# Performance work log

Measured on AMD Instinct MI355X. Metric: run time of the kernel, lower is better.

The kernel has to match this reference:

```python
import jax, jax.numpy as jnp
import numpy as np

N = 100000   # nodes
E = 1000000  # edges
F_IN = 128
H = 256
G = 64       # graphs in batch
EPS = 1e-5   # BatchNorm eps


def setup_inputs() -> dict:
    key = jax.random.key(0)
    ks = jax.random.split(key, 16)
    s = 0.05
    d = {}
    d["x"] = jax.random.normal(ks[0], (N, F_IN), jnp.float32)
    d["edge_index"] = jax.random.randint(ks[1], (2, E), 0, N, dtype=jnp.int32)
    d["batch"] = jnp.sort(jax.random.randint(ks[2], (N,), 0, G, dtype=jnp.int32))
    # block1 (128 -> 256, has projection)
    d["W1"] = jax.random.normal(ks[3], (F_IN, H), jnp.float32) * s
    d["b1"] = jnp.zeros((H,), jnp.float32)
    d["g1"] = jnp.ones((H,), jnp.float32)
    d["be1"] = jnp.zeros((H,), jnp.float32)
    d["P1"] = jax.random.normal(ks[4], (F_IN, H), jnp.float32) * s
    # blocks 2-4 (256 -> 256)
    for i, k in zip((2, 3, 4), (ks[5], ks[6], ks[7])):
        d[f"W{i}"] = jax.random.normal(k, (H, H), jnp.float32) * s
        d[f"b{i}"] = jnp.zeros((H,), jnp.float32)
        d[f"g{i}"] = jnp.ones((H,), jnp.float32)
        d[f"be{i}"] = jnp.zeros((H,), jnp.float32)
    d["Wl"] = jax.random.normal(ks[8], (H, 1), jnp.float32) * s
    d["bl"] = jnp.zeros((1,), jnp.float32)
    return d


def _gcn_norm(edge_index):
    # PyG gcn_norm: add self-loops, deg from dst column, norm = d^-1/2[src]*d^-1/2[dst]
    src, dst = edge_index[0], edge_index[1]
    deg = jax.ops.segment_sum(jnp.ones((E,), jnp.float32), dst, num_segments=N) + 1.0
    dis = jax.lax.rsqrt(deg)
    enorm = dis[src] * dis[dst]          # [E] normalization per edge
    self_w = 1.0 / deg                   # self-loop weight = deg^-1
    return src, dst, enorm, self_w


def _block(x, src, dst, enorm, self_w, W, b, g, be, P=None):
    hw = x @ W                                            # [N, H]
    msg = hw[src] * enorm[:, None]                        # [E, H] gather
    agg = jax.ops.segment_sum(msg, dst, num_segments=N)   # scatter-add
    agg = agg + hw * self_w[:, None] + b                  # self-loop + bias
    # BatchNorm1d (training-mode batch statistics, biased variance)
    m = jnp.mean(agg, axis=0)
    v = jnp.var(agg, axis=0)
    out = jax.nn.relu((agg - m) * jax.lax.rsqrt(v + EPS) * g + be)
    res = x @ P if P is not None else x
    return out + res


def reference(x, edge_index, batch, W1, b1, g1, be1, P1,
              W2, b2, g2, be2, W3, b3, g3, be3, W4, b4, g4, be4, Wl, bl):
    src, dst, enorm, self_w = _gcn_norm(edge_index)
    h = _block(x, src, dst, enorm, self_w, W1, b1, g1, be1, P1)
    h = _block(h, src, dst, enorm, self_w, W2, b2, g2, be2)
    h = _block(h, src, dst, enorm, self_w, W3, b3, g3, be3)
    h = _block(h, src, dst, enorm, self_w, W4, b4, g4, be4)
    # global mean pool over graphs
    sums = jax.ops.segment_sum(h, batch, num_segments=G)                       # [G, H]
    cnt = jax.ops.segment_sum(jnp.ones((N,), jnp.float32), batch, num_segments=G)
    pooled = sums / jnp.maximum(cnt, 1.0)[:, None]
    return pooled @ Wl + bl                                                    # [G, 1]
```

## Files before the change

kernel.cpp:

```cpp
#include <hip/hip_runtime.h>
#include <cstdint>
#include <cstddef>

#define NN 100000
#define NE 1000000
#define FIN 128
#define HD 256
#define NG 64
#define BNEPS 1e-5f

typedef unsigned short ushort_t;
typedef __attribute__((ext_vector_type(8))) short bf16x8;
typedef __attribute__((ext_vector_type(4))) float f32x4;


__device__ inline float b2f(unsigned short u) {
    union { float f; unsigned int i; } x; x.i = ((unsigned int)u) << 16; return x.f;
}
__device__ inline unsigned short f2b(float f) {
    union { float f; unsigned int i; } x; x.f = f;
    unsigned int r = x.i + 0x7FFFu + ((x.i >> 16) & 1u);
    return (unsigned short)(r >> 16);
}
__device__ inline float  ld1(const unsigned short* p) { return b2f(*p); }
__device__ inline float4 ld4v(const unsigned short* p) {
    ushort4 u = *(const ushort4*)p;
    return make_float4(b2f(u.x), b2f(u.y), b2f(u.z), b2f(u.w));
}
__device__ inline float2 ld2v(const unsigned short* p) {
    ushort2 u = *(const ushort2*)p;
    return make_float2(b2f(u.x), b2f(u.y));
}
__device__ inline void st4v(unsigned short* p, float4 v) {
    ushort4 u; u.x = f2b(v.x); u.y = f2b(v.y); u.z = f2b(v.z); u.w = f2b(v.w);
    *(ushort4*)p = u;
}
__device__ inline void st2v(unsigned short* p, float2 v) {
    ushort2 u; u.x = f2b(v.x); u.y = f2b(v.y);
    *(ushort2*)p = u;
}

__device__ inline void bn_sc_sh(float s, float q, float g, float be, float& sc, float& sh) {
    float m = s * (1.0f / NN);
    float v = q * (1.0f / NN) - m * m;
    sc = g * rsqrtf(v + BNEPS);
    sh = be - m * sc;
}


__global__ __launch_bounds__(256) void count_deg_k(const int* __restrict__ dst, int* __restrict__ cnt) {
    int e = blockIdx.x * 256 + threadIdx.x;
    if (e < NE) atomicAdd(&cnt[dst[e]], 1);
}

__global__ __launch_bounds__(256) void node_prep_k(const int* __restrict__ cnt,
                                                   float* __restrict__ dis, float* __restrict__ selfw) {
    int i = blockIdx.x * 256 + threadIdx.x;
    if (i < NN) {
        float d = (float)cnt[i] + 1.0f;
        dis[i] = rsqrtf(d);
        selfw[i] = 1.0f / d;
    }
}

__global__ __launch_bounds__(1024) void scan_reduce_k(const int* __restrict__ cnt, int* __restrict__ partials) {
    __shared__ int sh[1024];
    int i = blockIdx.x * 1024 + threadIdx.x;
    sh[threadIdx.x] = (i < NN) ? cnt[i] : 0;
    __syncthreads();
    for (int off = 512; off > 0; off >>= 1) {
        if (threadIdx.x < off) sh[threadIdx.x] += sh[threadIdx.x + off];
        __syncthreads();
    }
    if (threadIdx.x == 0) partials[blockIdx.x] = sh[0];
}

__global__ void scan_partials_k(int* partials, int nb) {
    if (threadIdx.x == 0 && blockIdx.x == 0) {
        int run = 0;
        for (int b = 0; b < nb; b++) { int v = partials[b]; partials[b] = run; run += v; }
    }
}

__global__ __launch_bounds__(1024) void scan_write_k(const int* __restrict__ cnt,
                                                     const int* __restrict__ partials,
                                                     int* __restrict__ rowptr) {
    __shared__ int sh[1024];
    int i = blockIdx.x * 1024 + threadIdx.x;
    int v = (i < NN) ? cnt[i] : 0;
    sh[threadIdx.x] = v;
    __syncthreads();
    for (int off = 1; off < 1024; off <<= 1) {
        int t = (threadIdx.x >= off) ? sh[threadIdx.x - off] : 0;
        __syncthreads();
        sh[threadIdx.x] += t;
        __syncthreads();
    }
    if (i < NN) rowptr[i] = partials[blockIdx.x] + sh[threadIdx.x] - v;
    if (i == NN - 1) rowptr[NN] = partials[blockIdx.x] + sh[threadIdx.x];
}

__global__ __launch_bounds__(256) void fill_csr_k(const int* __restrict__ src, const int* __restrict__ dst,
                                                  const int* __restrict__ rowptr, int* __restrict__ cursor,
                                                  const float* __restrict__ dis,
                                                  int2* __restrict__ csr) {
    int e = blockIdx.x * 256 + threadIdx.x;
    if (e < NE) {
        int d = dst[e], s = src[e];
        int pos = rowptr[d] + atomicAdd(&cursor[d], 1);
        float w = dis[s] * dis[d];
        csr[pos] = make_int2(s, __float_as_int(w));
    }
}

__global__ __launch_bounds__(256) void x2b_k(const float* __restrict__ x, unsigned short* __restrict__ xb) {
    int i = blockIdx.x * 256 + threadIdx.x;
    if (i < NN * FIN / 4) {
        float4 v = *reinterpret_cast<const float4*>(x + (size_t)i * 4);
        ushort4 u; u.x = f2b(v.x); u.y = f2b(v.y); u.z = f2b(v.z); u.w = f2b(v.w);
        *reinterpret_cast<ushort4*>(xb + (size_t)i * 4) = u;
    }
}

__global__ __launch_bounds__(256) void wt_all_k(const float* __restrict__ W1, const float* __restrict__ P1,
                                                const float* __restrict__ W2, const float* __restrict__ W3,
                                                const float* __restrict__ W4,
                                                unsigned short* __restrict__ w1t, unsigned short* __restrict__ p1t,
                                                unsigned short* __restrict__ w2t, unsigned short* __restrict__ w3t,
                                                unsigned short* __restrict__ w4t) {
    int b = blockIdx.x;
    const float* W; unsigned short* Bt; int K; int base;
    if (b < 128)      { W = W1; Bt = w1t; K = 128; base = b; }
    else if (b < 256) { W = P1; Bt = p1t; K = 128; base = b - 128; }
    else if (b < 512) { W = W2; Bt = w2t; K = 256; base = b - 256; }
    else if (b < 768) { W = W3; Bt = w3t; K = 256; base = b - 512; }
    else              { W = W4; Bt = w4t; K = 256; base = b - 768; }
    int i = base * 256 + threadIdx.x;
    if (i < K * 256) {
        int k = i >> 8, n = i & 255;
        Bt[n * K + k] = f2b(W[k * 256 + n]);
    }
}


template<int COLS>
__global__ __launch_bounds__(256) void spmm_k(const unsigned short* __restrict__ h,
                                              const int* __restrict__ rowptr,
                                              const int2* __restrict__ csr,
                                              const float* __restrict__ selfw,
                                              unsigned short* __restrict__ z) {
    const int lane = threadIdx.x & 63;
    const int row = blockIdx.x * 4 + (threadIdx.x >> 6);
    if (row >= NN) return;
    if constexpr (COLS == 256) {
        float4 a = ld4v(h + (size_t)row * COLS + lane * 4);
        float sw = selfw[row];
        float4 acc = make_float4(a.x * sw, a.y * sw, a.z * sw, a.w * sw);
        int e = rowptr[row];
        const int e1 = rowptr[row + 1];
        for (; e + 8 <= e1; e += 8) {
            int2 cc[8];
#pragma unroll
            for (int j = 0; j < 8; j++) cc[j] = csr[e + j];
            float4 hv[8];
#pragma unroll
            for (int j = 0; j < 8; j++) hv[j] = ld4v(h + (size_t)cc[j].x * COLS + lane * 4);
#pragma unroll
            for (int j = 0; j < 8; j++) {
                float w = __int_as_float(cc[j].y);
                acc.x += w * hv[j].x; acc.y += w * hv[j].y; acc.z += w * hv[j].z; acc.w += w * hv[j].w;
            }
        }
        for (; e + 4 <= e1; e += 4) {
            int2 c0 = csr[e], c1 = csr[e + 1], c2 = csr[e + 2], c3 = csr[e + 3];
            float4 h0 = ld4v(h + (size_t)c0.x * COLS + lane * 4);
            float4 h1 = ld4v(h + (size_t)c1.x * COLS + lane * 4);
            float4 h2 = ld4v(h + (size_t)c2.x * COLS + lane * 4);
            float4 h3 = ld4v(h + (size_t)c3.x * COLS + lane * 4);
            float w0 = __int_as_float(c0.y), w1 = __int_as_float(c1.y);
            float w2 = __int_as_float(c2.y), w3 = __int_as_float(c3.y);
            acc.x += w0 * h0.x; acc.y += w0 * h0.y; acc.z += w0 * h0.z; acc.w += w0 * h0.w;
            acc.x += w1 * h1.x; acc.y += w1 * h1.y; acc.z += w1 * h1.z; acc.w += w1 * h1.w;
            acc.x += w2 * h2.x; acc.y += w2 * h2.y; acc.z += w2 * h2.z; acc.w += w2 * h2.w;
            acc.x += w3 * h3.x; acc.y += w3 * h3.y; acc.z += w3 * h3.z; acc.w += w3 * h3.w;
        }
        for (; e < e1; e++) {
            int2 c = csr[e];
            float w = __int_as_float(c.y);
            float4 hv = ld4v(h + (size_t)c.x * COLS + lane * 4);
            acc.x += w * hv.x; acc.y += w * hv.y; acc.z += w * hv.z; acc.w += w * hv.w;
        }
        st4v(z + (size_t)row * COLS + lane * 4, acc);
    } else {
        float2 a = ld2v(h + (size_t)row * COLS + lane * 2);
        float sw = selfw[row];
        float2 acc = make_float2(a.x * sw, a.y * sw);
        int e = rowptr[row];
        const int e1 = rowptr[row + 1];
        for (; e + 8 <= e1; e += 8) {
            int2 cc[8];
#pragma unroll
            for (int j = 0; j < 8; j++) cc[j] = csr[e + j];
            float2 hv[8];
#pragma unroll
            for (int j = 0; j < 8; j++) hv[j] = ld2v(h + (size_t)cc[j].x * COLS + lane * 2);
#pragma unroll
            for (int j = 0; j < 8; j++) {
                float w = __int_as_float(cc[j].y);
                acc.x += w * hv[j].x; acc.y += w * hv[j].y;
            }
        }
        for (; e + 4 <= e1; e += 4) {
            int2 c0 = csr[e], c1 = csr[e + 1], c2 = csr[e + 2], c3 = csr[e + 3];
            float2 h0 = ld2v(h + (size_t)c0.x * COLS + lane * 2);
            float2 h1 = ld2v(h + (size_t)c1.x * COLS + lane * 2);
            float2 h2 = ld2v(h + (size_t)c2.x * COLS + lane * 2);
            float2 h3 = ld2v(h + (size_t)c3.x * COLS + lane * 2);
            float w0 = __int_as_float(c0.y), w1 = __int_as_float(c1.y);
            float w2 = __int_as_float(c2.y), w3 = __int_as_float(c3.y);
            acc.x += w0 * h0.x; acc.y += w0 * h0.y;
            acc.x += w1 * h1.x; acc.y += w1 * h1.y;
            acc.x += w2 * h2.x; acc.y += w2 * h2.y;
            acc.x += w3 * h3.x; acc.y += w3 * h3.y;
        }
        for (; e < e1; e++) {
            int2 c = csr[e];
            float w = __int_as_float(c.y);
            float2 hv = ld2v(h + (size_t)c.x * COLS + lane * 2);
            acc.x += w * hv.x; acc.y += w * hv.y;
        }
        st2v(z + (size_t)row * COLS + lane * 2, acc);
    }
}


#define RPB 391

template<int K, int MODE>
__global__ __launch_bounds__(1024, 4) void mgemm_k(const unsigned short* __restrict__ A,
                                                   const unsigned short* __restrict__ Bt,
                                                   const float* __restrict__ bias,
                                                   unsigned short* __restrict__ C,
                                                   const float* __restrict__ gamma,
                                                   const float* __restrict__ beta,
                                                   const float* __restrict__ sums_in,
                                                   const unsigned short* __restrict__ aggin,
                                                   float* __restrict__ sums_out, int M) {
    constexpr int NF = 8;
    constexpr int SEGS = K / 8;
    constexpr int KS = K / 32;
    __shared__ char Bl[256 * K * 2];
    __shared__ float sstat[512];
    const int tid  = threadIdx.x;
    const int lane = tid & 63;
    const int wid  = tid >> 6;
    const int wr   = wid & 7;
    const int cw   = wid >> 3;
    const int q    = lane >> 4;
    const int rl   = lane & 15;
    const int col0 = cw * 128;
    const int rbase = blockIdx.x * RPB;
    const int rend  = min(rbase + RPB, M);

    for (int s = tid; s < 256 * SEGS; s += 1024) {
        int col = s / SEGS, j = s % SEGS;
        uint4 v = *reinterpret_cast<const uint4*>(Bt + (size_t)col * K + j * 8);
        *reinterpret_cast<uint4*>(Bl + col * (K * 2) + ((j ^ (col & 7)) << 4)) = v;
    }
    if (MODE == 0 && tid < 512) sstat[tid] = 0.f;
    __syncthreads();

    for (int it = 0; it < 2; it++) {
        const int row0 = rbase + it * 256 + wr * 32;
        if (row0 >= rend) continue;

        const int a0r = min(row0 + rl, M - 1);
        const int a1r = min(row0 + 16 + rl, M - 1);
        const unsigned short* pa0 = A + (size_t)a0r * K + q * 8;
        const unsigned short* pa1 = A + (size_t)a1r * K + q * 8;

        f32x4 acc[2][NF];
#pragma unroll
        for (int m = 0; m < 2; m++)
#pragma unroll
            for (int n = 0; n < NF; n++) acc[m][n] = (f32x4){0.f, 0.f, 0.f, 0.f};

#pragma unroll
        for (int ks = 0; ks < KS; ks++) {
            bf16x8 af0 = *reinterpret_cast<const bf16x8*>(pa0 + ks * 32);
            bf16x8 af1 = *reinterpret_cast<const bf16x8*>(pa1 + ks * 32);
#pragma unroll
            for (int nf = 0; nf < NF; nf++) {
                int colL = col0 + nf * 16 + rl;
                bf16x8 bf = *reinterpret_cast<const bf16x8*>(Bl + colL * (K * 2) + (((ks * 4 + q) ^ (colL & 7)) << 4));
                acc[0][nf] = __builtin_amdgcn_mfma_f32_16x16x32_bf16(bf, af0, acc[0][nf], 0, 0, 0);
                acc[1][nf] = __builtin_amdgcn_mfma_f32_16x16x32_bf16(bf, af1, acc[1][nf], 0, 0, 0);
            }
        }

        const int g0 = row0 + rl, g1 = row0 + 16 + rl;
        const bool ok0 = g0 < rend, ok1 = g1 < rend;
#pragma unroll
        for (int nf = 0; nf < NF; nf++) {
            int cb = col0 + nf * 16 + q * 4;
            f32x4 v0 = acc[0][nf], v1 = acc[1][nf];
            if (MODE == 0) {
                float4 bb = *reinterpret_cast<const float4*>(bias + cb);
                v0[0] += bb.x; v0[1] += bb.y; v0[2] += bb.z; v0[3] += bb.w;
                v1[0] += bb.x; v1[1] += bb.y; v1[2] += bb.z; v1[3] += bb.w;
            } else {
                float4 s4 = *reinterpret_cast<const float4*>(sums_in + cb);
                float4 q4 = *reinterpret_cast<const float4*>(sums_in + 256 + cb);
                float4 gm = *reinterpret_cast<const float4*>(gamma + cb);
                float4 bt = *reinterpret_cast<const float4*>(beta + cb);
                float sc[4], sh[4];
                bn_sc_sh(s4.x, q4.x, gm.x, bt.x, sc[0], sh[0]);
                bn_sc_sh(s4.y, q4.y, gm.y, bt.y, sc[1], sh[1]);
                bn_sc_sh(s4.z, q4.z, gm.z, bt.z, sc[2], sh[2]);
                bn_sc_sh(s4.w, q4.w, gm.w, bt.w, sc[3], sh[3]);
                if (ok0) {
                    ushort4 ag = *reinterpret_cast<const ushort4*>(aggin + (size_t)g0 * HD + cb);
                    v0[0] += fmaxf(fmaf(b2f(ag.x), sc[0], sh[0]), 0.f);
                    v0[1] += fmaxf(fmaf(b2f(ag.y), sc[1], sh[1]), 0.f);
                    v0[2] += fmaxf(fmaf(b2f(ag.z), sc[2], sh[2]), 0.f);
                    v0[3] += fmaxf(fmaf(b2f(ag.w), sc[3], sh[3]), 0.f);
                }
                if (ok1) {
                    ushort4 ag = *reinterpret_cast<const ushort4*>(aggin + (size_t)g1 * HD + cb);
                    v1[0] += fmaxf(fmaf(b2f(ag.x), sc[0], sh[0]), 0.f);
                    v1[1] += fmaxf(fmaf(b2f(ag.y), sc[1], sh[1]), 0.f);
                    v1[2] += fmaxf(fmaf(b2f(ag.z), sc[2], sh[2]), 0.f);
                    v1[3] += fmaxf(fmaf(b2f(ag.w), sc[3], sh[3]), 0.f);
                }
            }
            if (ok0) {
                ushort4 u; u.x = f2b(v0[0]); u.y = f2b(v0[1]); u.z = f2b(v0[2]); u.w = f2b(v0[3]);
                *reinterpret_cast<ushort4*>(C + (size_t)g0 * HD + cb) = u;
            }
            if (ok1) {
                ushort4 u; u.x = f2b(v1[0]); u.y = f2b(v1[1]); u.z = f2b(v1[2]); u.w = f2b(v1[3]);
                *reinterpret_cast<ushort4*>(C + (size_t)g1 * HD + cb) = u;
            }
            if (MODE == 0) {
                if (!ok0) { v0[0] = v0[1] = v0[2] = v0[3] = 0.f; }
                if (!ok1) { v1[0] = v1[1] = v1[2] = v1[3] = 0.f; }
                float s[4], qq[4];
#pragma unroll
                for (int j = 0; j < 4; j++) {
                    s[j]  = v0[j] + v1[j];
                    qq[j] = v0[j] * v0[j] + v1[j] * v1[j];
                }
#pragma unroll
                for (int m = 1; m < 16; m <<= 1) {
#pragma unroll
                    for (int j = 0; j < 4; j++) {
                        s[j]  += __shfl_xor(s[j], m, 64);
                        qq[j] += __shfl_xor(qq[j], m, 64);
                    }
                }
                if (rl == 0) {
#pragma unroll
                    for (int j = 0; j < 4; j++) {
                        atomicAdd(&sstat[cb + j], s[j]);
                        atomicAdd(&sstat[256 + cb + j], qq[j]);
                    }
                }
            }
        }
    }

    if (MODE == 0) {
        __syncthreads();
        if (tid < 512) atomicAdd(&sums_out[tid], sstat[tid]);
    }
}


__global__ __launch_bounds__(256) void epi_k(const unsigned short* __restrict__ agg,
                                             const unsigned short* __restrict__ res,
                                             const float* __restrict__ sums,
                                             const float* __restrict__ gamma,
                                             const float* __restrict__ beta,
                                             unsigned short* __restrict__ out) {
    const size_t total = (size_t)NN * (HD / 4);
    size_t i = (size_t)blockIdx.x * 256 + threadIdx.x;
    const size_t stride = (size_t)gridDim.x * 256;
    for (; i < total; i += stride) {
        int cq = ((int)(i & 63)) * 4;
        float4 a = ld4v(agg + i * 4);
        float4 r = ld4v(res + i * 4);
        float4 s4 = *reinterpret_cast<const float4*>(sums + cq);
        float4 q4 = *reinterpret_cast<const float4*>(sums + 256 + cq);
        float4 gm = *reinterpret_cast<const float4*>(gamma + cq);
        float4 bt = *reinterpret_cast<const float4*>(beta + cq);
        float sc0, sh0, sc1, sh1, sc2, sh2, sc3, sh3;
        bn_sc_sh(s4.x, q4.x, gm.x, bt.x, sc0, sh0);
        bn_sc_sh(s4.y, q4.y, gm.y, bt.y, sc1, sh1);
        bn_sc_sh(s4.z, q4.z, gm.z, bt.z, sc2, sh2);
        bn_sc_sh(s4.w, q4.w, gm.w, bt.w, sc3, sh3);
        float4 o;
        o.x = fmaxf(fmaf(a.x, sc0, sh0), 0.f) + r.x;
        o.y = fmaxf(fmaf(a.y, sc1, sh1), 0.f) + r.y;
        o.z = fmaxf(fmaf(a.z, sc2, sh2), 0.f) + r.z;
        o.w = fmaxf(fmaf(a.w, sc3, sh3), 0.f) + r.w;
        st4v(out + i * 4, o);
    }
}


#define EP_RPB 40

__global__ __launch_bounds__(256) void epi_pool_k(const unsigned short* __restrict__ lin,
                                                  const unsigned short* __restrict__ res,
                                                  const float* __restrict__ sums,
                                                  const float* __restrict__ gamma,
                                                  const float* __restrict__ beta,
                                                  const int* __restrict__ batch,
                                                  float* __restrict__ pooled) {
    const int c = threadIdx.x;
    const int rs = blockIdx.x * EP_RPB;
    if (rs >= NN) return;
    const int re = min(rs + EP_RPB, NN);
    float sc, sh;
    bn_sc_sh(sums[c], sums[256 + c], gamma[c], beta[c], sc, sh);
    float acc = 0.f;
    int cur = batch[rs];
    int r = rs;
    for (; r + 4 <= re; r += 4) {
        float a[4], rr[4]; int g[4];
#pragma unroll
        for (int j = 0; j < 4; j++) {
            a[j]  = b2f(lin[(size_t)(r + j) * HD + c]);
            rr[j] = b2f(res[(size_t)(r + j) * HD + c]);
            g[j]  = batch[r + j];
        }
#pragma unroll
        for (int j = 0; j < 4; j++) {
            if (g[j] != cur) { atomicAdd(&pooled[(size_t)cur * HD + c], acc); acc = 0.f; cur = g[j]; }
            acc += fmaxf(fmaf(a[j], sc, sh), 0.f) + rr[j];
        }
    }
    for (; r < re; r++) {
        int g = batch[r];
        if (g != cur) { atomicAdd(&pooled[(size_t)cur * HD + c], acc); acc = 0.f; cur = g; }
        float a = b2f(lin[(size_t)r * HD + c]);
        float rv = b2f(res[(size_t)r * HD + c]);
        acc += fmaxf(fmaf(a, sc, sh), 0.f) + rv;
    }
    atomicAdd(&pooled[(size_t)cur * HD + c], acc);
}

__global__ void pool_out_k(const float* __restrict__ pooled, const int* __restrict__ batch,
                           const float* __restrict__ Wl, const float* __restrict__ bl,
                           float* __restrict__ out) {
    int g = threadIdx.x;
    if (g < NG) {
        auto lb = [&](int val) {
            int lo = 0, hi = NN;
            while (lo < hi) { int mid = (lo + hi) >> 1; if (batch[mid] < val) lo = mid + 1; else hi = mid; }
            return lo;
        };
        int c0 = lb(g), c1 = lb(g + 1);
        float cn = fmaxf((float)(c1 - c0), 1.0f);
        float s = 0.f;
        for (int c = 0; c < HD; c++) s += pooled[(size_t)g * HD + c] * Wl[c];
        out[g] = s / cn + bl[0];
    }
}


static inline size_t alignup(size_t x) { return (x + 255) & ~size_t(255); }

extern "C" void kernel_launch(void* const* d_in, const int* in_sizes, int n_in,
                              void* d_out, int out_size, void* d_ws, size_t ws_size,
                              hipStream_t stream) {
    const float* x    = (const float*)d_in[0];
    const int*   ei   = (const int*)d_in[1];
    const int*   bat  = (const int*)d_in[2];
    const float* W1   = (const float*)d_in[3];
    const float* bi1  = (const float*)d_in[4];
    const float* g1   = (const float*)d_in[5];
    const float* be1  = (const float*)d_in[6];
    const float* P1   = (const float*)d_in[7];
    const float* W2   = (const float*)d_in[8];
    const float* bi2  = (const float*)d_in[9];
    const float* g2   = (const float*)d_in[10];
    const float* be2  = (const float*)d_in[11];
    const float* W3   = (const float*)d_in[12];
    const float* bi3  = (const float*)d_in[13];
    const float* g3   = (const float*)d_in[14];
    const float* be3  = (const float*)d_in[15];
    const float* W4   = (const float*)d_in[16];
    const float* bi4  = (const float*)d_in[17];
    const float* g4   = (const float*)d_in[18];
    const float* be4  = (const float*)d_in[19];
    const float* Wl   = (const float*)d_in[20];
    const float* bl   = (const float*)d_in[21];
    float* out = (float*)d_out;

    const int* e_src = ei;
    const int* e_dst = ei + NE;

    typedef unsigned short ST;
    char* p = (char*)d_ws;
    auto alloc = [&](size_t bytes) { char* q = p; p += alignup(bytes); return q; };
    ST*    fb0     = (ST*)alloc((size_t)NN * HD * sizeof(ST));
    ST*    fb1     = (ST*)alloc((size_t)NN * HD * sizeof(ST));
    ST*    fb2     = (ST*)alloc((size_t)NN * HD * sizeof(ST));
    ST*    xb      = (ST*)alloc((size_t)NN * FIN * sizeof(ST));
    float* dis     = (float*)alloc((size_t)NN * 4);
    float* selfw   = (float*)alloc((size_t)NN * 4);
    int*   rowptr  = (int*)alloc((size_t)(NN + 1) * 4);
    int2*  csr     = (int2*)alloc((size_t)NE * 8);
    int*   partials= (int*)alloc(128 * 4);
    ST*    w1t     = (ST*)alloc(256 * 128 * sizeof(ST));
    ST*    p1t     = (ST*)alloc(256 * 128 * sizeof(ST));
    ST*    w2t     = (ST*)alloc(256 * 256 * sizeof(ST));
    ST*    w3t     = (ST*)alloc(256 * 256 * sizeof(ST));
    ST*    w4t     = (ST*)alloc(256 * 256 * sizeof(ST));
    size_t zbytes = (size_t)NN * 4 + (size_t)NN * 4 + 4 * 2 * HD * 4 + (size_t)NG * HD * 4;
    char*  zbase   = alloc(zbytes);
    int*   cnt     = (int*)zbase;
    int*   cursor  = (int*)(zbase + (size_t)NN * 4);
    float* sums1   = (float*)(zbase + (size_t)NN * 8);
    float* sums2   = sums1 + 2 * HD;
    float* sums3   = sums2 + 2 * HD;
    float* sums4   = sums3 + 2 * HD;
    float* pooled  = sums4 + 2 * HD;

    const int NB = (NN + 1023) / 1024;

    hipMemsetAsync(zbase, 0, zbytes, stream);

    wt_all_k<<<1024, 256, 0, stream>>>(W1, P1, W2, W3, W4, w1t, p1t, w2t, w3t, w4t);
    x2b_k<<<(NN * FIN / 4 + 255) / 256, 256, 0, stream>>>(x, xb);

    count_deg_k<<<(NE + 255) / 256, 256, 0, stream>>>(e_dst, cnt);
    node_prep_k<<<(NN + 255) / 256, 256, 0, stream>>>(cnt, dis, selfw);
    scan_reduce_k<<<NB, 1024, 0, stream>>>(cnt, partials);
    scan_partials_k<<<1, 64, 0, stream>>>(partials, NB);
    scan_write_k<<<NB, 1024, 0, stream>>>(cnt, partials, rowptr);
    fill_csr_k<<<(NE + 255) / 256, 256, 0, stream>>>(e_src, e_dst, rowptr, cursor, dis, csr);

    spmm_k<128><<<NN / 4, 256, 0, stream>>>(xb, rowptr, csr, selfw, fb0);
    mgemm_k<128, 0><<<256, 1024, 0, stream>>>(fb0, w1t, bi1, fb2, nullptr, nullptr, nullptr, nullptr, sums1, NN);
    mgemm_k<128, 1><<<256, 1024, 0, stream>>>(xb, p1t, nullptr, fb1, g1, be1, sums1, fb2, nullptr, NN);

    spmm_k<256><<<NN / 4, 256, 0, stream>>>(fb1, rowptr, csr, selfw, fb0);
    mgemm_k<256, 0><<<256, 1024, 0, stream>>>(fb0, w2t, bi2, fb2, nullptr, nullptr, nullptr, nullptr, sums2, NN);
    epi_k<<<4096, 256, 0, stream>>>(fb2, fb1, sums2, g2, be2, fb0);

    spmm_k<256><<<NN / 4, 256, 0, stream>>>(fb0, rowptr, csr, selfw, fb1);
    mgemm_k<256, 0><<<256, 1024, 0, stream>>>(fb1, w3t, bi3, fb2, nullptr, nullptr, nullptr, nullptr, sums3, NN);
    epi_k<<<4096, 256, 0, stream>>>(fb2, fb0, sums3, g3, be3, fb1);

    spmm_k<256><<<NN / 4, 256, 0, stream>>>(fb1, rowptr, csr, selfw, fb0);
    mgemm_k<256, 0><<<256, 1024, 0, stream>>>(fb0, w4t, bi4, fb2, nullptr, nullptr, nullptr, nullptr, sums4, NN);
    epi_pool_k<<<(NN + EP_RPB - 1) / EP_RPB, 256, 0, stream>>>(fb2, fb1, sums4, g4, be4, bat, pooled);
    pool_out_k<<<1, 64, 0, stream>>>(pooled, bat, Wl, bl, out);
}
```

Baseline: 757.1 us.

## Split GEMM column halves across a 2D grid and parallelize partials scan

```diff
diff --git a/kernel.cpp b/kernel.cpp
--- a/kernel.cpp
+++ b/kernel.cpp
@@ -75,11 +75,19 @@
     if (threadIdx.x == 0) partials[blockIdx.x] = sh[0];
 }
 
-__global__ void scan_partials_k(int* partials, int nb) {
-    if (threadIdx.x == 0 && blockIdx.x == 0) {
-        int run = 0;
-        for (int b = 0; b < nb; b++) { int v = partials[b]; partials[b] = run; run += v; }
-    }
+__global__ __launch_bounds__(128) void scan_partials_k(int* partials, int nb) {
+    __shared__ int sh[128];
+    int t = threadIdx.x;
+    int v = (t < nb) ? partials[t] : 0;
+    sh[t] = v;
+    __syncthreads();
+    for (int off = 1; off < 128; off <<= 1) {
+        int u = (t >= off) ? sh[t - off] : 0;
+        __syncthreads();
+        sh[t] += u;
+        __syncthreads();
+    }
+    if (t < nb) partials[t] = sh[t] - v;
 }
 
 __global__ __launch_bounds__(1024) void scan_write_k(const int* __restrict__ cnt,
@@ -237,41 +245,40 @@
 #define RPB 391
 
 template<int K, int MODE>
-__global__ __launch_bounds__(1024, 4) void mgemm_k(const unsigned short* __restrict__ A,
-                                                   const unsigned short* __restrict__ Bt,
-                                                   const float* __restrict__ bias,
-                                                   unsigned short* __restrict__ C,
-                                                   const float* __restrict__ gamma,
-                                                   const float* __restrict__ beta,
-                                                   const float* __restrict__ sums_in,
-                                                   const unsigned short* __restrict__ aggin,
-                                                   float* __restrict__ sums_out, int M) {
-    constexpr int NF = 8;
+__global__ __launch_bounds__(512, 4) void mgemm_k(const unsigned short* __restrict__ A,
+                                                  const unsigned short* __restrict__ Bt,
+                                                  const float* __restrict__ bias,
+                                                  unsigned short* __restrict__ C,
+                                                  const float* __restrict__ gamma,
+                                                  const float* __restrict__ beta,
+                                                  const float* __restrict__ sums_in,
+                                                  const unsigned short* __restrict__ aggin,
+                                                  float* __restrict__ sums_out, int M) {
+    constexpr int NCOLS = 128;
+    constexpr int NF = NCOLS / 16;
     constexpr int SEGS = K / 8;
     constexpr int KS = K / 32;
-    __shared__ char Bl[256 * K * 2];
-    __shared__ float sstat[512];
+    __shared__ char Bl[NCOLS * K * 2];
+    __shared__ float sstat[2 * NCOLS];
     const int tid  = threadIdx.x;
     const int lane = tid & 63;
     const int wid  = tid >> 6;
-    const int wr   = wid & 7;
-    const int cw   = wid >> 3;
     const int q    = lane >> 4;
     const int rl   = lane & 15;
-    const int col0 = cw * 128;
+    const int col0 = blockIdx.y * NCOLS;
     const int rbase = blockIdx.x * RPB;
     const int rend  = min(rbase + RPB, M);
 
-    for (int s = tid; s < 256 * SEGS; s += 1024) {
+    for (int s = tid; s < NCOLS * SEGS; s += 512) {
         int col = s / SEGS, j = s % SEGS;
-        uint4 v = *reinterpret_cast<const uint4*>(Bt + (size_t)col * K + j * 8);
+        uint4 v = *reinterpret_cast<const uint4*>(Bt + (size_t)(col0 + col) * K + j * 8);
         *reinterpret_cast<uint4*>(Bl + col * (K * 2) + ((j ^ (col & 7)) << 4)) = v;
     }
-    if (MODE == 0 && tid < 512) sstat[tid] = 0.f;
+    if (MODE == 0 && tid < 2 * NCOLS) sstat[tid] = 0.f;
     __syncthreads();
 
     for (int it = 0; it < 2; it++) {
-        const int row0 = rbase + it * 256 + wr * 32;
+        const int row0 = rbase + it * 256 + wid * 32;
         if (row0 >= rend) continue;
 
         const int a0r = min(row0 + rl, M - 1);
@@ -291,8 +298,8 @@
             bf16x8 af1 = *reinterpret_cast<const bf16x8*>(pa1 + ks * 32);
 #pragma unroll
             for (int nf = 0; nf < NF; nf++) {
-                int colL = col0 + nf * 16 + rl;
-                bf16x8 bf = *reinterpret_cast<const bf16x8*>(Bl + colL * (K * 2) + (((ks * 4 + q) ^ (colL & 7)) << 4));
+                int col = nf * 16 + rl;
+                bf16x8 bf = *reinterpret_cast<const bf16x8*>(Bl + col * (K * 2) + (((ks * 4 + q) ^ (col & 7)) << 4));
                 acc[0][nf] = __builtin_amdgcn_mfma_f32_16x16x32_bf16(bf, af0, acc[0][nf], 0, 0, 0);
                 acc[1][nf] = __builtin_amdgcn_mfma_f32_16x16x32_bf16(bf, af1, acc[1][nf], 0, 0, 0);
             }
@@ -359,10 +366,11 @@
                     }
                 }
                 if (rl == 0) {
+                    int cl = nf * 16 + q * 4;
 #pragma unroll
                     for (int j = 0; j < 4; j++) {
-                        atomicAdd(&sstat[cb + j], s[j]);
-                        atomicAdd(&sstat[256 + cb + j], qq[j]);
+                        atomicAdd(&sstat[cl + j], s[j]);
+                        atomicAdd(&sstat[NCOLS + cl + j], qq[j]);
                     }
                 }
             }
@@ -371,7 +379,8 @@
 
     if (MODE == 0) {
         __syncthreads();
-        if (tid < 512) atomicAdd(&sums_out[tid], sstat[tid]);
+        if (tid < NCOLS)            atomicAdd(&sums_out[col0 + tid], sstat[tid]);
+        else if (tid < 2 * NCOLS)   atomicAdd(&sums_out[256 + col0 + (tid - NCOLS)], sstat[tid]);
     }
 }
 
@@ -529,6 +538,7 @@
     float* pooled  = sums4 + 2 * HD;
 
     const int NB = (NN + 1023) / 1024;
+    dim3 gg(256, 2);
 
     hipMemsetAsync(zbase, 0, zbytes, stream);
 
@@ -538,24 +548,24 @@
     count_deg_k<<<(NE + 255) / 256, 256, 0, stream>>>(e_dst, cnt);
     node_prep_k<<<(NN + 255) / 256, 256, 0, stream>>>(cnt, dis, selfw);
     scan_reduce_k<<<NB, 1024, 0, stream>>>(cnt, partials);
-    scan_partials_k<<<1, 64, 0, stream>>>(partials, NB);
+    scan_partials_k<<<1, 128, 0, stream>>>(partials, NB);
     scan_write_k<<<NB, 1024, 0, stream>>>(cnt, partials, rowptr);
     fill_csr_k<<<(NE + 255) / 256, 256, 0, stream>>>(e_src, e_dst, rowptr, cursor, dis, csr);
 
     spmm_k<128><<<NN / 4, 256, 0, stream>>>(xb, rowptr, csr, selfw, fb0);
-    mgemm_k<128, 0><<<256, 1024, 0, stream>>>(fb0, w1t, bi1, fb2, nullptr, nullptr, nullptr, nullptr, sums1, NN);
-    mgemm_k<128, 1><<<256, 1024, 0, stream>>>(xb, p1t, nullptr, fb1, g1, be1, sums1, fb2, nullptr, NN);
+    mgemm_k<128, 0><<<gg, 512, 0, stream>>>(fb0, w1t, bi1, fb2, nullptr, nullptr, nullptr, nullptr, sums1, NN);
+    mgemm_k<128, 1><<<gg, 512, 0, stream>>>(xb, p1t, nullptr, fb1, g1, be1, sums1, fb2, nullptr, NN);
 
     spmm_k<256><<<NN / 4, 256, 0, stream>>>(fb1, rowptr, csr, selfw, fb0);
-    mgemm_k<256, 0><<<256, 1024, 0, stream>>>(fb0, w2t, bi2, fb2, nullptr, nullptr, nullptr, nullptr, sums2, NN);
+    mgemm_k<256, 0><<<gg, 512, 0, stream>>>(fb0, w2t, bi2, fb2, nullptr, nullptr, nullptr, nullptr, sums2, NN);
     epi_k<<<4096, 256, 0, stream>>>(fb2, fb1, sums2, g2, be2, fb0);
 
     spmm_k<256><<<NN / 4, 256, 0, stream>>>(fb0, rowptr, csr, selfw, fb1);
-    mgemm_k<256, 0><<<256, 1024, 0, stream>>>(fb1, w3t, bi3, fb2, nullptr, nullptr, nullptr, nullptr, sums3, NN);
+    mgemm_k<256, 0><<<gg, 512, 0, stream>>>(fb1, w3t, bi3, fb2, nullptr, nullptr, nullptr, nullptr, sums3, NN);
     epi_k<<<4096, 256, 0, stream>>>(fb2, fb0, sums3, g3, be3, fb1);
 
     spmm_k<256><<<NN / 4, 256, 0, stream>>>(fb1, rowptr, csr, selfw, fb0);
-    mgemm_k<256, 0><<<256, 1024, 0, stream>>>(fb0, w4t, bi4, fb2, nullptr, nullptr, nullptr, nullptr, sums4, NN);
+    mgemm_k<256, 0><<<gg, 512, 0, stream>>>(fb0, w4t, bi4, fb2, nullptr, nullptr, nullptr, nullptr, sums4, NN);
     epi_pool_k<<<(NN + EP_RPB - 1) / EP_RPB, 256, 0, stream>>>(fb2, fb1, sums4, g4, be4, bat, pooled);
     pool_out_k<<<1, 64, 0, stream>>>(pooled, bat, Wl, bl, out);
 }
```

Result: no change. 746.2 us (-1.4%).
